# Optimization experiments

Measured on AMD Instinct MI355X. Metric: run time of the kernel, lower is better.

The kernel has to match this reference:

```python
import jax, jax.numpy as jnp
import numpy as np

R = 6  # displacement radius -> (2R+1)^2 = 169 displacements


def setup_inputs() -> dict:
    key = jax.random.key(0)
    k1, k2, k3, k4, k5 = jax.random.split(key, 5)
    B, C, H, W = 4, 64, 256, 256
    s = 0.05  # scale so softmax over 128-dim dot products is not saturated
    return {
        "feats_r": jax.random.normal(k1, (B, C, H, W), jnp.float32) * s,
        "feats_t": jax.random.normal(k2, (B, C, H, W), jnp.float32) * s,
        "img_r": jax.random.uniform(k3, (B, 1, H, W), jnp.float32),
        "plf_1": jax.random.normal(k4, (B, C, H, W), jnp.float32) * s,
        "plf_2": jax.random.normal(k5, (B, C, H, W), jnp.float32) * s,
    }


def reference(feats_r, feats_t, img_r, plf_1, plf_2):
    # train_mode=True: concat pseudo-label features along channel dim
    x1 = jnp.concatenate([feats_t, plf_1], axis=1)   # [B, 2C, H, W] (query)
    x2 = jnp.concatenate([feats_r, plf_2], axis=1)   # [B, 2C, H, W] (reference)
    x2p = jnp.pad(x2, ((0, 0), (0, 0), (R, R), (R, R)))
    imgp = jnp.pad(img_r, ((0, 0), (0, 0), (R, R), (R, R)))

    D = 2 * R + 1
    # displacement order matches the original nested loops: _y outer, _x inner
    dy, dx = jnp.meshgrid(jnp.arange(D), jnp.arange(D), indexing="ij")
    disp = jnp.stack([dy.reshape(-1), dx.reshape(-1)], axis=-1)  # [D^2, 2]

    x1_shape = x1.shape
    img_shape = img_r.shape

    def step(carry, d):
        oy, ox = d[0], d[1]
        win = jax.lax.dynamic_slice(x2p, (0, 0, oy, ox), x1_shape)      # [B,2C,H,W]
        corr = jnp.sum(x1 * win, axis=1)                                 # [B,H,W]
        iw = jax.lax.dynamic_slice(imgp, (0, 0, oy, ox), img_shape)      # [B,c,H,W]
        return carry, (corr, iw)

    _, (corr, imgw) = jax.lax.scan(step, None, disp)
    # corr: [D^2, B, H, W]; imgw: [D^2, B, c, H, W]
    soft = jax.nn.softmax(corr, axis=0)
    # img_t[b,c,h,w] = sum_d soft[d,b,h,w] * imgw[d,b,c,h,w]
    img_t = jnp.einsum("dbhw,dbchw->bchw", soft, imgw)
    return img_t
```

## Files before the change

### kernel.cpp

```cpp
#include <hip/hip_runtime.h>

typedef float    float4v __attribute__((ext_vector_type(4)));
typedef float4v  float4u __attribute__((aligned(4)));
typedef _Float16 f16x2   __attribute__((ext_vector_type(2)));
typedef _Float16 f16x4   __attribute__((ext_vector_type(4)));
typedef _Float16 f16x8   __attribute__((ext_vector_type(8)));

#if defined(__has_builtin)
#  if __has_builtin(__builtin_amdgcn_fdot2)
#    define USE_FDOT2 1
#  else
#    define USE_FDOT2 0
#  endif
#  if __has_builtin(__builtin_amdgcn_cvt_pkrtz)
#    define USE_PKRTZ 1
#  else
#    define USE_PKRTZ 0
#  endif
#else
#  define USE_FDOT2 0
#  define USE_PKRTZ 0
#endif

__device__ __forceinline__ float fdot2f(f16x2 a, f16x2 b, float c) {
#if USE_FDOT2
    return __builtin_amdgcn_fdot2(a, b, c, false);
#else
    return fmaf((float)a[1], (float)b[1], fmaf((float)a[0], (float)b[0], c));
#endif
}
__device__ __forceinline__ f16x2 pk2(float x, float y) {
#if USE_PKRTZ
    return __builtin_bit_cast(f16x2, __builtin_amdgcn_cvt_pkrtz(x, y));
#else
    return (f16x2){(_Float16)x, (_Float16)y};
#endif
}

__global__ __launch_bounds__(256, 2)
void corr_soft_warp(const float* __restrict__ feats_r,
                    const float* __restrict__ feats_t,
                    const float* __restrict__ img_r,
                    const float* __restrict__ plf_1,
                    const float* __restrict__ plf_2,
                    float* __restrict__ out)
{
    constexpr int W = 256;
    constexpr int NPIX = 256 * 256;
    __shared__ __align__(16) f16x2    stg[4][8][272];
    __shared__ __align__(16) _Float16 pc2[13][4][256];

    const int bid     = (int)blockIdx.x;
    const int logical = (bid & 7) * 128 + (bid >> 3);
    const int b = logical >> 8;
    const int h = logical & 255;

    const int tid  = (int)threadIdx.x;
    const int cs   = tid >> 6;
    const int lane = tid & 63;
    const int w0   = lane << 2;

    const size_t plane = (size_t)NPIX;
    const float* __restrict__ x1arr = ((cs < 2) ? feats_t : plf_1) + (size_t)b * 64 * plane;
    const float* __restrict__ x2arr = ((cs < 2) ? feats_r : plf_2) + (size_t)b * 64 * plane;
    const float* __restrict__ img   = img_r + (size_t)b * plane;
    const int cl0 = (cs & 1) << 5;

    f16x2 x1r[4][16];
    {
        const float* p0 = x1arr + (size_t)cl0 * plane + (size_t)h * W + w0;
        #pragma unroll
        for (int cp = 0; cp < 16; ++cp) {
            float4v a = *(const float4v*)(p0 + (size_t)(2 * cp) * plane);
            float4v c = *(const float4v*)(p0 + (size_t)(2 * cp + 1) * plane);
            #pragma unroll
            for (int pix = 0; pix < 4; ++pix)
                x1r[pix][cp] = pk2(a[pix], c[pix]);
        }
    }

    const int p = tid;
    float m = -1e30f, lsum = 0.f, acc = 0.f;

    #pragma unroll 1
    for (int dy = 0; dy < 13; ++dy) {
        const int row = h + dy - 6;
        const bool inRow = ((unsigned)row < 256u);
        float s[13], iw[13];

        if (inRow) {
            float corr[4][13];
            #pragma unroll
            for (int pix = 0; pix < 4; ++pix)
                #pragma unroll
                for (int dx = 0; dx < 13; ++dx) corr[pix][dx] = 0.f;

            const float* rbase = x2arr + (size_t)cl0 * plane + (size_t)row * W;

            #pragma unroll
            for (int ph = 0; ph < 2; ++ph) {
                #pragma unroll
                for (int cpl = 0; cpl < 8; ++cpl) {
                    const int cp = ph * 8 + cpl;
                    const float* r0 = rbase + (size_t)(2 * cp) * plane;
                    const float* r1 = r0 + plane;
                    #pragma unroll
                    for (int xq = 0; xq < 2; ++xq) {
                        const int q = xq ? (64 + lane) : lane;
                        const bool active = (xq == 0) | (lane < 3);
                        if (active) {
                            const int gq = 4 * q - 6;
                            float4v A, B;
                            if (gq >= 0 && gq <= 252) {
                                A = *(const float4u*)(r0 + gq);
                                B = *(const float4u*)(r1 + gq);
                            } else {
                                #pragma unroll
                                for (int k = 0; k < 4; ++k) {
                                    const int cc = gq + k;
                                    const bool ok = ((unsigned)cc < 256u);
                                    A[k] = ok ? r0[cc] : 0.f;
                                    B[k] = ok ? r1[cc] : 0.f;
                                }
                            }
                            f16x8 e;
                            #pragma unroll
                            for (int k = 0; k < 4; ++k) {
                                f16x2 t = pk2(A[k], B[k]);
                                e[2 * k]     = t[0];
                                e[2 * k + 1] = t[1];
                            }
                            *(f16x8*)&stg[cs][cpl][q << 2] = e;
                        }
                    }
                }
                #pragma unroll
                for (int cpl = 0; cpl < 8; ++cpl) {
                    const int cp = ph * 8 + cpl;
                    union { f16x8 v8; f16x2 v2[4]; } Q[4];
                    #pragma unroll
                    for (int mq = 0; mq < 4; ++mq)
                        Q[mq].v8 = *(const f16x8*)&stg[cs][cpl][w0 + (mq << 2)];
                    #pragma unroll
                    for (int pix = 0; pix < 4; ++pix) {
                        const f16x2 xv = x1r[pix][cp];
                        #pragma unroll
                        for (int dx = 0; dx < 13; ++dx) {
                            const int u = pix + dx;
                            corr[pix][dx] = fdot2f(xv, Q[u >> 2].v2[u & 3], corr[pix][dx]);
                        }
                    }
                }
            }
            #pragma unroll
            for (int dx = 0; dx < 13; ++dx) {
                f16x4 v = {(_Float16)corr[0][dx], (_Float16)corr[1][dx],
                           (_Float16)corr[2][dx], (_Float16)corr[3][dx]};
                *(f16x4*)&pc2[dx][cs][w0] = v;
            }
        }
        __syncthreads();

        if (inRow) {
            const float* imrow = img + (size_t)row * W;
            #pragma unroll
            for (int dx = 0; dx < 13; ++dx) {
                s[dx] = ((float)pc2[dx][0][p] + (float)pc2[dx][1][p])
                      + ((float)pc2[dx][2][p] + (float)pc2[dx][3][p]);
                const int col = p + dx - 6;
                iw[dx] = ((unsigned)col < 256u) ? imrow[col] : 0.f;
            }
        } else {
            #pragma unroll
            for (int dx = 0; dx < 13; ++dx) { s[dx] = 0.f; iw[dx] = 0.f; }
        }
        __syncthreads();

        float mloc = s[0];
        #pragma unroll
        for (int dx = 1; dx < 13; ++dx) mloc = fmaxf(mloc, s[dx]);
        const float mn = fmaxf(m, mloc);
        const float scale = __expf(m - mn);
        lsum *= scale; acc *= scale;
        #pragma unroll
        for (int dx = 0; dx < 13; ++dx) {
            const float e = __expf(s[dx] - mn);
            lsum += e;
            acc = fmaf(e, iw[dx], acc);
        }
        m = mn;
    }

    out[(size_t)b * plane + (size_t)h * W + p] = acc / lsum;
}

extern "C" void kernel_launch(void* const* d_in, const int* in_sizes, int n_in,
                              void* d_out, int out_size, void* d_ws, size_t ws_size,
                              hipStream_t stream) {
    const float* feats_r = (const float*)d_in[0];
    const float* feats_t = (const float*)d_in[1];
    const float* img_r   = (const float*)d_in[2];
    const float* plf_1   = (const float*)d_in[3];
    const float* plf_2   = (const float*)d_in[4];
    float* outp = (float*)d_out;

    corr_soft_warp<<<dim3(1024), dim3(256), 0, stream>>>(
        feats_r, feats_t, img_r, plf_1, plf_2, outp);
}
```

Before: 857.8 us.

## Shrink LDS staging to one channel pair and prefetch next pair in registers

```diff
diff --git a/kernel.cpp b/kernel.cpp
--- a/kernel.cpp
+++ b/kernel.cpp
@@ -37,7 +37,7 @@
 #endif
 }
 
-__global__ __launch_bounds__(256, 2)
+__global__ __launch_bounds__(256, 3)
 void corr_soft_warp(const float* __restrict__ feats_r,
                     const float* __restrict__ feats_t,
                     const float* __restrict__ img_r,
@@ -47,7 +47,7 @@
 {
     constexpr int W = 256;
     constexpr int NPIX = 256 * 256;
-    __shared__ __align__(16) f16x2    stg[4][8][272];
+    __shared__ __align__(16) f16x2    stg[4][272];
     __shared__ __align__(16) _Float16 pc2[13][4][256];
 
     const int bid     = (int)blockIdx.x;
@@ -82,6 +82,10 @@
     const int p = tid;
     float m = -1e30f, lsum = 0.f, acc = 0.f;
 
+    const int gq0  = (lane << 2) - 6;
+    const int gq1  = ((64 + lane) << 2) - 6;
+    const bool act1 = (lane < 3);
+
     #pragma unroll 1
     for (int dy = 0; dy < 13; ++dy) {
         const int row = h + dy - 6;
@@ -89,68 +93,72 @@
         float s[13], iw[13];
 
         if (inRow) {
+            const float* rbase = x2arr + (size_t)cl0 * plane + (size_t)row * W;
+
+            auto loadq = [&](const float* r, int gq) -> float4v {
+                if (gq >= 0 && gq <= 252) return *(const float4u*)(r + gq);
+                float4v v;
+                #pragma unroll
+                for (int k = 0; k < 4; ++k) {
+                    const int cc = gq + k;
+                    v[k] = ((unsigned)cc < 256u) ? r[cc] : 0.f;
+                }
+                return v;
+            };
+            auto loadstage = [&](int c, float4v& A0, float4v& B0,
+                                 float4v& A1, float4v& B1) {
+                const float* r0 = rbase + (size_t)(2 * c) * plane;
+                const float* r1 = r0 + plane;
+                A0 = loadq(r0, gq0);
+                B0 = loadq(r1, gq0);
+                if (act1) { A1 = loadq(r0, gq1); B1 = loadq(r1, gq1); }
+            };
+
             float corr[4][13];
             #pragma unroll
             for (int pix = 0; pix < 4; ++pix)
                 #pragma unroll
                 for (int dx = 0; dx < 13; ++dx) corr[pix][dx] = 0.f;
 
-            const float* rbase = x2arr + (size_t)cl0 * plane + (size_t)row * W;
-
-            #pragma unroll
-            for (int ph = 0; ph < 2; ++ph) {
-                #pragma unroll
-                for (int cpl = 0; cpl < 8; ++cpl) {
-                    const int cp = ph * 8 + cpl;
-                    const float* r0 = rbase + (size_t)(2 * cp) * plane;
-                    const float* r1 = r0 + plane;
+            float4v cA0, cB0, cA1, cB1, nA0, nB0, nA1, nB1;
+            loadstage(0, cA0, cB0, cA1, cB1);
+
+            #pragma unroll
+            for (int c = 0; c < 16; ++c) {
+                if (c < 15) loadstage(c + 1, nA0, nB0, nA1, nB1);
+
+                {
+                    f16x8 e;
                     #pragma unroll
-                    for (int xq = 0; xq < 2; ++xq) {
-                        const int q = xq ? (64 + lane) : lane;
-                        const bool active = (xq == 0) | (lane < 3);
-                        if (active) {
-                            const int gq = 4 * q - 6;
-                            float4v A, B;
-                            if (gq >= 0 && gq <= 252) {
-                                A = *(const float4u*)(r0 + gq);
-                                B = *(const float4u*)(r1 + gq);
-                            } else {
-                                #pragma unroll
-                                for (int k = 0; k < 4; ++k) {
-                                    const int cc = gq + k;
-                                    const bool ok = ((unsigned)cc < 256u);
-                                    A[k] = ok ? r0[cc] : 0.f;
-                                    B[k] = ok ? r1[cc] : 0.f;
-                                }
-                            }
-                            f16x8 e;
-                            #pragma unroll
-                            for (int k = 0; k < 4; ++k) {
-                                f16x2 t = pk2(A[k], B[k]);
-                                e[2 * k]     = t[0];
-                                e[2 * k + 1] = t[1];
-                            }
-                            *(f16x8*)&stg[cs][cpl][q << 2] = e;
+                    for (int k = 0; k < 4; ++k) {
+                        f16x2 t = pk2(cA0[k], cB0[k]);
+                        e[2 * k] = t[0]; e[2 * k + 1] = t[1];
+                    }
+                    *(f16x8*)&stg[cs][lane << 2] = e;
+                    if (act1) {
+                        f16x8 e1;
+                        #pragma unroll
+                        for (int k = 0; k < 4; ++k) {
+                            f16x2 t = pk2(cA1[k], cB1[k]);
+                            e1[2 * k] = t[0]; e1[2 * k + 1] = t[1];
                         }
+                        *(f16x8*)&stg[cs][(64 + lane) << 2] = e1;
                     }
                 }
-                #pragma unroll
-                for (int cpl = 0; cpl < 8; ++cpl) {
-                    const int cp = ph * 8 + cpl;
-                    union { f16x8 v8; f16x2 v2[4]; } Q[4];
+                union { f16x8 v8; f16x2 v2[4]; } Q[4];
+                #pragma unroll
+                for (int mq = 0; mq < 4; ++mq)
+                    Q[mq].v8 = *(const f16x8*)&stg[cs][w0 + (mq << 2)];
+                #pragma unroll
+                for (int pix = 0; pix < 4; ++pix) {
+                    const f16x2 xv = x1r[pix][c];
                     #pragma unroll
-                    for (int mq = 0; mq < 4; ++mq)
-                        Q[mq].v8 = *(const f16x8*)&stg[cs][cpl][w0 + (mq << 2)];
-                    #pragma unroll
-                    for (int pix = 0; pix < 4; ++pix) {
-                        const f16x2 xv = x1r[pix][cp];
-                        #pragma unroll
-                        for (int dx = 0; dx < 13; ++dx) {
-                            const int u = pix + dx;
-                            corr[pix][dx] = fdot2f(xv, Q[u >> 2].v2[u & 3], corr[pix][dx]);
-                        }
+                    for (int dx = 0; dx < 13; ++dx) {
+                        const int u = pix + dx;
+                        corr[pix][dx] = fdot2f(xv, Q[u >> 2].v2[u & 3], corr[pix][dx]);
                     }
                 }
+                cA0 = nA0; cB0 = nB0; cA1 = nA1; cB1 = nB1;
             }
             #pragma unroll
             for (int dx = 0; dx < 13; ++dx) {
```

After: 2.121 ms. 2.47x slower.
